# Performance work log

Measured on AMD Instinct MI355X. Metric: run time of the kernel, lower is better.

## Reference

```python
import jax, jax.numpy as jnp
import numpy as np

B, T, F, H, P = 256, 512, 64, 512, 24  # batch, seq_len, fea_dim, hidden, pred_sequence


def setup_inputs() -> dict:
    key = jax.random.key(0)
    ks = jax.random.split(key, 7)
    s = 1.0 / np.sqrt(H)  # PyTorch default init scale
    u = lambda k, shp: jax.random.uniform(k, shp, jnp.float32, -s, s)
    return {
        "x": jax.random.normal(ks[0], (B, T, F), jnp.float32),
        "W_ih": u(ks[1], (4 * H, F)),
        "W_hh": u(ks[2], (4 * H, H)),
        "b_ih": u(ks[3], (4 * H,)),
        "b_hh": u(ks[4], (4 * H,)),
        "W_fc": u(ks[5], (P * F, H)),
        "b_fc": u(ks[6], (P * F,)),
    }


def reference(x, W_ih, W_hh, b_ih, b_hh, W_fc, b_fc):
    b, t, f = x.shape
    h4 = W_hh.shape[1]
    # Precompute input contribution to gates for all timesteps: [B,T,4H]
    x_gates = jnp.einsum('btf,gf->btg', x, W_ih) + b_ih + b_hh

    def step(carry, xg):  # xg: [B,4H]
        h, c = carry
        gates = xg + h @ W_hh.T  # [B,4H]
        i, fg, g, o = jnp.split(gates, 4, axis=-1)  # PyTorch gate order i,f,g,o
        i = jax.nn.sigmoid(i)
        fg = jax.nn.sigmoid(fg)
        o = jax.nn.sigmoid(o)
        g = jnp.tanh(g)
        c = fg * c + i * g
        h = o * jnp.tanh(c)
        return (h, c), None

    h0 = jnp.zeros((b, h4), x.dtype)
    c0 = jnp.zeros((b, h4), x.dtype)
    (hn, cn), _ = jax.lax.scan(step, (h0, c0), jnp.swapaxes(x_gates, 0, 1))
    # hn.squeeze() for num_layers=1 -> [B,H]; fc head then reshape to [B,P,F]
    out = hn @ W_fc.T + b_fc
    return out.reshape(-1, P, f)
```

## Files before the change

### kernel.cpp

```cpp
#include <hip/hip_runtime.h>
#include <stdint.h>


namespace {
constexpr int T_STEPS = 512;
constexpr int FEA  = 64;
constexpr int HID  = 512;
constexpr int NKI  = 18;
constexpr int GSTR = 132;
constexpr int RPG  = 16;
constexpr int GPITCH = 136;
constexpr size_t HBUF_DW  = 256ull * 256;
constexpr size_t FLAG_OFF = 2 * HBUF_DW;
constexpr size_t GRZ_OFF  = FLAG_OFF + 16 * 64;

typedef __bf16   bf16x8 __attribute__((ext_vector_type(8)));
typedef uint16_t u16x8  __attribute__((ext_vector_type(8)));
typedef float    f32x4  __attribute__((ext_vector_type(4)));
typedef uint32_t u32x4  __attribute__((ext_vector_type(4)));

union V8 { u16x8 u; bf16x8 b; u32x4 q; };

__device__ __forceinline__ float bf2f(uint16_t u) {
  union { uint32_t i; float f; } v; v.i = (uint32_t)u << 16; return v.f;
}
__device__ __forceinline__ uint16_t f2bf(float f) {
  union { float f; uint32_t i; } v; v.f = f;
  uint32_t x = v.i;
  return (uint16_t)((x + 0x7FFFu + ((x >> 16) & 1u)) >> 16);
}
__device__ __forceinline__ float sigmoid_f(float x) {
  return 1.0f / (1.0f + __expf(-x));
}
__device__ __forceinline__ float tanh_f(float x) {
  float e = __expf(-2.0f * fabsf(x));
  float t = (1.0f - e) / (1.0f + e);
  return copysignf(t, x);
}
__device__ __forceinline__ bf16x8 load8(const void* base, size_t elem_off,
                                        bool fp32m) {
  V8 r;
  if (fp32m) {
    const float* p = (const float*)base + elem_off;
#pragma unroll
    for (int i = 0; i < 8; ++i) r.u[i] = f2bf(p[i]);
  } else {
    r.q = *(const u32x4*)((const uint16_t*)base + elem_off);
  }
  return r.b;
}
__device__ __forceinline__ float loadf(const void* base, int idx, bool fp32m) {
  return fp32m ? ((const float*)base)[idx] : bf2f(((const uint16_t*)base)[idx]);
}
__device__ __forceinline__ uint2 ldx4(const void* x, size_t elem_off,
                                      bool fp32m) {
  if (fp32m) {
    float4 v = *(const float4*)((const float*)x + elem_off);
    uint2 w;
    w.x = (uint32_t)f2bf(v.x) | ((uint32_t)f2bf(v.y) << 16);
    w.y = (uint32_t)f2bf(v.z) | ((uint32_t)f2bf(v.w) << 16);
    return w;
  }
  return *(const uint2*)((const uint16_t*)x + elem_off);
}

__device__ __forceinline__ u32x4 ld128_sc01(const uint32_t* p) {
  u32x4 v;
  asm volatile("global_load_dwordx4 %0, %1, off sc0 sc1"
               : "=v"(v) : "v"(p) : "memory");
  return v;
}
__device__ __forceinline__ void st32_x(uint32_t* p, uint32_t v, bool xl) {
  if (xl) asm volatile("global_store_dword %0, %1, off sc0"
                       :: "v"(p), "v"(v) : "memory");
  else    asm volatile("global_store_dword %0, %1, off sc0 sc1"
                       :: "v"(p), "v"(v) : "memory");
}
__device__ __forceinline__ void waitcnt_vm0() {
  asm volatile("s_waitcnt vmcnt(0)" ::: "memory");
}
__device__ __forceinline__ void waitcnt_vm0_fence() {
  asm volatile("s_waitcnt vmcnt(0)" ::: "memory");
  __builtin_amdgcn_sched_barrier(0);
}
}

__global__ __launch_bounds__(256, 1) void lstm_persistent(
    const void* __restrict__ x,
    const void* __restrict__ W_ih,
    const void* __restrict__ W_hh,
    const void* __restrict__ b_ih,
    const void* __restrict__ b_hh,
    const void* __restrict__ W_fc,
    const void* __restrict__ b_fc,
    void* __restrict__ out,
    uint32_t* __restrict__ dbuf)
{
  __shared__ __align__(16) uint16_t Als[72 * GPITCH];
  __shared__ float Gls[RPG * GSTR];
  __shared__ int   sflag, sok;

  const int tid = threadIdx.x;
  const int wv  = tid >> 6;
  const int ln  = tid & 63;
  const int nl  = ln & 15;
  const int kq  = ln >> 4;
  const int bg  = blockIdx.x & 15;
  const int wgi = blockIdx.x >> 4;
  const int r0  = bg * RPG;

  if (tid == 0) {
    uint32_t xcc;
    asm volatile("s_getreg_b32 %0, hwreg(HW_REG_XCC_ID)" : "=s"(xcc));
    unsigned* gmask = (unsigned*)(dbuf + GRZ_OFF) + bg;
    unsigned* gcnt  = (unsigned*)(dbuf + GRZ_OFF) + 16 + bg;
    atomicOr(gmask, 1u << (xcc & 31));
    __threadfence();
    atomicAdd(gcnt, 1u);
    while (atomicAdd(gcnt, 0u) < 16u) __builtin_amdgcn_s_sleep(1);
    __threadfence();
    unsigned m = atomicOr(gmask, 0u);
    sok = (__popc(m) == 1) ? 1 : 0;
  }

  if (tid == 1) sflag = 0;
  __syncthreads();
  {
    float a = fabsf(bf2f(((const uint16_t*)b_ih)[tid]));
    if (a > 1.0f) atomicOr(&sflag, 1);
  }
  __syncthreads();
  const bool fp32m = (sflag != 0);
  const bool xloc  = (sok != 0);

  bf16x8 breg[2][NKI];
  float  bias[2];
#pragma unroll
  for (int s = 0; s < 2; ++s) {
    int col  = wv * 32 + s * 16 + nl;
    int gate = col & 3;
    int unit = col >> 2;
    int gcol = gate * HID + wgi * 32 + unit;
#pragma unroll
    for (int kk = 0; kk < NKI; ++kk) {
      int k0 = kk * 32 + kq * 8;
      if (k0 < HID)
        breg[s][kk] = load8(W_hh, (size_t)gcol * HID + k0, fp32m);
      else
        breg[s][kk] = load8(W_ih, (size_t)gcol * FEA + (k0 - HID), fp32m);
    }
    bias[s] = loadf(b_ih, gcol, fp32m) + loadf(b_hh, gcol, fp32m);
  }

  const int ar  = tid >> 4;
  const int au  = (tid & 15) * 2;
  const int hdw = (r0 + ar) * 256 + wgi * 16 + (tid & 15);
  float c0 = 0.0f, c1 = 0.0f;

  const int srow = tid >> 4;
  const int sc   = tid & 15;

  uint32_t* flagw = dbuf + FLAG_OFF + bg * 64 + wgi * 4 + wv;
  const uint32_t* fb0 = dbuf + FLAG_OFF + bg * 64;

  {
    u32x4 z = {0, 0, 0, 0};
    for (int i = tid; i < 64 * GPITCH / 8; i += 256)
      *(u32x4*)&Als[i * 8] = z;
  }
  {
    int gx = sc & 7, hf = sc >> 3;
    size_t off = (size_t)(r0 + srow) * (T_STEPS * FEA) + gx * 8 + hf * 4;
    uint2 w = ldx4(x, off, fp32m);
    *(uint2*)&Als[(64 + gx) * GPITCH + srow * 8 + hf * 4] = w;
  }

  for (int t = 0; t < T_STEPS; ++t) {
    __syncthreads();

    f32x4 acc0, acc1;
    acc0[0] = bias[0]; acc0[1] = bias[0]; acc0[2] = bias[0]; acc0[3] = bias[0];
    acc1[0] = bias[1]; acc1[1] = bias[1]; acc1[2] = bias[1]; acc1[3] = bias[1];
#pragma unroll
    for (int kk = 0; kk < NKI; ++kk) {
      bf16x8 a = *(const bf16x8*)&Als[(4 * kk + kq) * GPITCH + nl * 8];
      acc0 = __builtin_amdgcn_mfma_f32_16x16x32_bf16(a, breg[0][kk], acc0, 0, 0, 0);
      acc1 = __builtin_amdgcn_mfma_f32_16x16x32_bf16(a, breg[1][kk], acc1, 0, 0, 0);
    }
#pragma unroll
    for (int r = 0; r < 4; ++r) {
      Gls[(kq * 4 + r) * GSTR + wv * 32 + nl]      = acc0[r];
      Gls[(kq * 4 + r) * GSTR + wv * 32 + 16 + nl] = acc1[r];
    }
    __syncthreads();

    const uint32_t tg = (uint32_t)(t + 1);
    const bool havex = (t + 1 < T_STEPS);

    {
      const f32x4* gp = (const f32x4*)&Gls[ar * GSTR + au * 4];
      f32x4 ga = gp[0], gb = gp[1];
      c0 = sigmoid_f(ga[1]) * c0 + sigmoid_f(ga[0]) * tanh_f(ga[2]);
      float h0 = sigmoid_f(ga[3]) * tanh_f(c0);
      c1 = sigmoid_f(gb[1]) * c1 + sigmoid_f(gb[0]) * tanh_f(gb[2]);
      float h1 = sigmoid_f(gb[3]) * tanh_f(c1);
      uint32_t hp = (uint32_t)f2bf(h0) | ((uint32_t)f2bf(h1) << 16);
      st32_x(dbuf + (size_t)(tg & 1) * HBUF_DW + hdw, hp, xloc);
      waitcnt_vm0();
      if (ln == 0) st32_x(flagw, tg, xloc);
    }

    if (havex) {
      int gx = sc & 7, hf = sc >> 3;
      size_t off = (size_t)(r0 + srow) * (T_STEPS * FEA)
                 + (size_t)(t + 1) * FEA + gx * 8 + hf * 4;
      uint2 w = ldx4(x, off, fp32m);
      *(uint2*)&Als[(64 + gx) * GPITCH + srow * 8 + hf * 4] = w;
    }

    if (tid < 16) {
      const uint32_t* fp = fb0 + tid * 4;
      for (;;) {
        u32x4 f = ld128_sc01(fp);
        waitcnt_vm0_fence();
        uint32_t mn = f[0];
        mn = f[1] < mn ? f[1] : mn;
        mn = f[2] < mn ? f[2] : mn;
        mn = f[3] < mn ? f[3] : mn;
        if (mn >= tg) break;
      }
    }
    __syncthreads();

    if (havex) {
      const uint32_t* src = dbuf + (size_t)(tg & 1) * HBUF_DW
                          + (size_t)(r0 + srow) * 256;
      u32x4 v0 = ld128_sc01(src + (sc + 0)  * 4);
      u32x4 v1 = ld128_sc01(src + (sc + 16) * 4);
      u32x4 v2 = ld128_sc01(src + (sc + 32) * 4);
      u32x4 v3 = ld128_sc01(src + (sc + 48) * 4);
      waitcnt_vm0();
      *(u32x4*)&Als[(sc + 0)  * GPITCH + srow * 8] = v0;
      *(u32x4*)&Als[(sc + 16) * GPITCH + srow * 8] = v1;
      *(u32x4*)&Als[(sc + 32) * GPITCH + srow * 8] = v2;
      *(u32x4*)&Als[(sc + 48) * GPITCH + srow * 8] = v3;
    }
  }

  int gwave = wgi * 4 + wv;
  for (int tile = gwave; tile < 96; tile += 64) {
    int n = tile * 16 + nl;
    float bs = loadf(b_fc, n, fp32m);
    f32x4 acc; acc[0] = bs; acc[1] = bs; acc[2] = bs; acc[3] = bs;
    const uint32_t* hb = dbuf + (size_t)(r0 + nl) * 256 + kq * 4;
    V8 av[16];
#pragma unroll
    for (int p = 0; p < 16; ++p) av[p].q = ld128_sc01(hb + p * 16);
    waitcnt_vm0_fence();
#pragma unroll
    for (int kk = 0; kk < 16; ++kk) {
      bf16x8 b = load8(W_fc, (size_t)n * HID + kk * 32 + kq * 8, fp32m);
      acc = __builtin_amdgcn_mfma_f32_16x16x32_bf16(av[kk].b, b, acc, 0, 0, 0);
    }
#pragma unroll
    for (int r = 0; r < 4; ++r) {
      int row = r0 + kq * 4 + r;
      if (fp32m) ((float*)out)[(size_t)row * 1536 + n] = acc[r];
      else       ((uint16_t*)out)[(size_t)row * 1536 + n] = f2bf(acc[r]);
    }
  }
}

extern "C" void kernel_launch(void* const* d_in, const int* in_sizes, int n_in,
                              void* d_out, int out_size, void* d_ws, size_t ws_size,
                              hipStream_t stream) {
  const void* x    = d_in[0];
  const void* W_ih = d_in[1];
  const void* W_hh = d_in[2];
  const void* b_ih = d_in[3];
  const void* b_hh = d_in[4];
  const void* W_fc = d_in[5];
  const void* b_fc = d_in[6];
  uint32_t* dbuf = (uint32_t*)d_ws;

  hipMemsetAsync((void*)(dbuf + FLAG_OFF), 0,
                 (16 * 64 + 32) * sizeof(uint32_t), stream);

  lstm_persistent<<<dim3(256), dim3(256), 0, stream>>>(
      x, W_ih, W_hh, b_ih, b_hh, W_fc, b_fc, d_out, dbuf);
}
```

Measured before the change: 1.033 ms.

## Per-lane flag polling with direct h-chunk fetch; split MFMA accumulators; fc reads LDS

Result: slower. 1.170 ms (+13.2%).

```diff
diff --git a/kernel.cpp b/kernel.cpp
--- a/kernel.cpp
+++ b/kernel.cpp
@@ -64,6 +64,12 @@
   return *(const uint2*)((const uint16_t*)x + elem_off);
 }
 
+__device__ __forceinline__ uint32_t ld32_sc01(const uint32_t* p) {
+  uint32_t v;
+  asm volatile("global_load_dword %0, %1, off sc0 sc1"
+               : "=v"(v) : "v"(p) : "memory");
+  return v;
+}
 __device__ __forceinline__ u32x4 ld128_sc01(const uint32_t* p) {
   u32x4 v;
   asm volatile("global_load_dwordx4 %0, %1, off sc0 sc1"
@@ -160,8 +166,12 @@
   const int srow = tid >> 4;
   const int sc   = tid & 15;
 
+  const int prow = ln & 15;
+  const int pkk  = wv * 4 + (ln >> 4);
+
   uint32_t* flagw = dbuf + FLAG_OFF + bg * 64 + wgi * 4 + wv;
   const uint32_t* fb0 = dbuf + FLAG_OFF + bg * 64;
+  const uint32_t* pflag = fb0 + pkk * 4 + (prow >> 2);
 
   {
     u32x4 z = {0, 0, 0, 0};
@@ -178,19 +188,27 @@
   for (int t = 0; t < T_STEPS; ++t) {
     __syncthreads();
 
-    f32x4 acc0, acc1;
-    acc0[0] = bias[0]; acc0[1] = bias[0]; acc0[2] = bias[0]; acc0[3] = bias[0];
-    acc1[0] = bias[1]; acc1[1] = bias[1]; acc1[2] = bias[1]; acc1[3] = bias[1];
+    f32x4 c0a, c0b, c1a, c1b;
+#pragma unroll
+    for (int i = 0; i < 4; ++i) {
+      c0a[i] = bias[0]; c1a[i] = bias[1]; c0b[i] = 0.0f; c1b[i] = 0.0f;
+    }
 #pragma unroll
     for (int kk = 0; kk < NKI; ++kk) {
       bf16x8 a = *(const bf16x8*)&Als[(4 * kk + kq) * GPITCH + nl * 8];
-      acc0 = __builtin_amdgcn_mfma_f32_16x16x32_bf16(a, breg[0][kk], acc0, 0, 0, 0);
-      acc1 = __builtin_amdgcn_mfma_f32_16x16x32_bf16(a, breg[1][kk], acc1, 0, 0, 0);
-    }
+      if (kk & 1) {
+        c0b = __builtin_amdgcn_mfma_f32_16x16x32_bf16(a, breg[0][kk], c0b, 0, 0, 0);
+        c1b = __builtin_amdgcn_mfma_f32_16x16x32_bf16(a, breg[1][kk], c1b, 0, 0, 0);
+      } else {
+        c0a = __builtin_amdgcn_mfma_f32_16x16x32_bf16(a, breg[0][kk], c0a, 0, 0, 0);
+        c1a = __builtin_amdgcn_mfma_f32_16x16x32_bf16(a, breg[1][kk], c1a, 0, 0, 0);
+      }
+    }
+    f32x4 A0 = c0a + c0b, A1 = c1a + c1b;
 #pragma unroll
     for (int r = 0; r < 4; ++r) {
-      Gls[(kq * 4 + r) * GSTR + wv * 32 + nl]      = acc0[r];
-      Gls[(kq * 4 + r) * GSTR + wv * 32 + 16 + nl] = acc1[r];
+      Gls[(kq * 4 + r) * GSTR + wv * 32 + nl]      = A0[r];
+      Gls[(kq * 4 + r) * GSTR + wv * 32 + 16 + nl] = A1[r];
     }
     __syncthreads();
 
@@ -218,49 +236,38 @@
       *(uint2*)&Als[(64 + gx) * GPITCH + srow * 8 + hf * 4] = w;
     }
 
-    if (tid < 16) {
-      const uint32_t* fp = fb0 + tid * 4;
+    {
       for (;;) {
-        u32x4 f = ld128_sc01(fp);
+        uint32_t f = ld32_sc01(pflag);
         waitcnt_vm0_fence();
-        uint32_t mn = f[0];
-        mn = f[1] < mn ? f[1] : mn;
-        mn = f[2] < mn ? f[2] : mn;
-        mn = f[3] < mn ? f[3] : mn;
-        if (mn >= tg) break;
+        if (f >= tg) break;
       }
-    }
-    __syncthreads();
-
-    if (havex) {
       const uint32_t* src = dbuf + (size_t)(tg & 1) * HBUF_DW
-                          + (size_t)(r0 + srow) * 256;
-      u32x4 v0 = ld128_sc01(src + (sc + 0)  * 4);
-      u32x4 v1 = ld128_sc01(src + (sc + 16) * 4);
-      u32x4 v2 = ld128_sc01(src + (sc + 32) * 4);
-      u32x4 v3 = ld128_sc01(src + (sc + 48) * 4);
+                          + (size_t)(r0 + prow) * 256 + pkk * 16;
+      u32x4 v0 = ld128_sc01(src + 0);
+      u32x4 v1 = ld128_sc01(src + 4);
+      u32x4 v2 = ld128_sc01(src + 8);
+      u32x4 v3 = ld128_sc01(src + 12);
       waitcnt_vm0();
-      *(u32x4*)&Als[(sc + 0)  * GPITCH + srow * 8] = v0;
-      *(u32x4*)&Als[(sc + 16) * GPITCH + srow * 8] = v1;
-      *(u32x4*)&Als[(sc + 32) * GPITCH + srow * 8] = v2;
-      *(u32x4*)&Als[(sc + 48) * GPITCH + srow * 8] = v3;
-    }
-  }
+      uint16_t* d = &Als[(pkk * 4) * GPITCH + prow * 8];
+      *(u32x4*)(d + 0 * GPITCH) = v0;
+      *(u32x4*)(d + 1 * GPITCH) = v1;
+      *(u32x4*)(d + 2 * GPITCH) = v2;
+      *(u32x4*)(d + 3 * GPITCH) = v3;
+    }
+  }
+  __syncthreads();
 
   int gwave = wgi * 4 + wv;
   for (int tile = gwave; tile < 96; tile += 64) {
     int n = tile * 16 + nl;
     float bs = loadf(b_fc, n, fp32m);
     f32x4 acc; acc[0] = bs; acc[1] = bs; acc[2] = bs; acc[3] = bs;
-    const uint32_t* hb = dbuf + (size_t)(r0 + nl) * 256 + kq * 4;
-    V8 av[16];
-#pragma unroll
-    for (int p = 0; p < 16; ++p) av[p].q = ld128_sc01(hb + p * 16);
-    waitcnt_vm0_fence();
 #pragma unroll
     for (int kk = 0; kk < 16; ++kk) {
+      bf16x8 a = *(const bf16x8*)&Als[(4 * kk + kq) * GPITCH + nl * 8];
       bf16x8 b = load8(W_fc, (size_t)n * HID + kk * 32 + kq * 8, fp32m);
-      acc = __builtin_amdgcn_mfma_f32_16x16x32_bf16(av[kk].b, b, acc, 0, 0, 0);
+      acc = __builtin_amdgcn_mfma_f32_16x16x32_bf16(a, b, acc, 0, 0, 0);
     }
 #pragma unroll
     for (int r = 0; r < 4; ++r) {
```

## Double-buffer LDS A tile and drop per-step block barriers in LSTM recurrence

Applied to the files above, without the earlier changes.

Result: faster. 1.003 ms (-3.0%).

```diff
diff --git a/kernel.cpp b/kernel.cpp
--- a/kernel.cpp
+++ b/kernel.cpp
@@ -7,8 +7,7 @@
 constexpr int FEA  = 64;
 constexpr int HID  = 512;
 constexpr int NKI  = 18;
-constexpr int GSTR = 132;
-constexpr int RPG  = 16;
+constexpr int GWS  = 36;
 constexpr int GPITCH = 136;
 constexpr size_t HBUF_DW  = 256ull * 256;
 constexpr size_t FLAG_OFF = 2 * HBUF_DW;
@@ -64,6 +63,12 @@
   return *(const uint2*)((const uint16_t*)x + elem_off);
 }
 
+__device__ __forceinline__ uint32_t ld32_sc01(const uint32_t* p) {
+  uint32_t v;
+  asm volatile("global_load_dword %0, %1, off sc0 sc1"
+               : "=v"(v) : "v"(p) : "memory");
+  return v;
+}
 __device__ __forceinline__ u32x4 ld128_sc01(const uint32_t* p) {
   u32x4 v;
   asm volatile("global_load_dwordx4 %0, %1, off sc0 sc1"
@@ -96,8 +101,8 @@
     void* __restrict__ out,
     uint32_t* __restrict__ dbuf)
 {
-  __shared__ __align__(16) uint16_t Als[72 * GPITCH];
-  __shared__ float Gls[RPG * GSTR];
+  __shared__ __align__(16) uint16_t Als[2][72 * GPITCH];
+  __shared__ float Gw[4][16 * GWS];
   __shared__ int   sflag, sok;
 
   const int tid = threadIdx.x;
@@ -107,7 +112,7 @@
   const int kq  = ln >> 4;
   const int bg  = blockIdx.x & 15;
   const int wgi = blockIdx.x >> 4;
-  const int r0  = bg * RPG;
+  const int r0  = bg * 16;
 
   if (tid == 0) {
     uint32_t xcc;
@@ -152,54 +157,59 @@
     bias[s] = loadf(b_ih, gcol, fp32m) + loadf(b_hh, gcol, fp32m);
   }
 
-  const int ar  = tid >> 4;
-  const int au  = (tid & 15) * 2;
-  const int hdw = (r0 + ar) * 256 + wgi * 16 + (tid & 15);
+  const int arow = ln >> 2;
+  const int up   = ln & 3;
+  const int hdw  = (r0 + arow) * 256 + wgi * 16 + wv * 4 + up;
   float c0 = 0.0f, c1 = 0.0f;
 
   const int srow = tid >> 4;
   const int sc   = tid & 15;
 
   uint32_t* flagw = dbuf + FLAG_OFF + bg * 64 + wgi * 4 + wv;
-  const uint32_t* fb0 = dbuf + FLAG_OFF + bg * 64;
+  const uint32_t* fbase = dbuf + FLAG_OFF + bg * 64;
 
   {
     u32x4 z = {0, 0, 0, 0};
     for (int i = tid; i < 64 * GPITCH / 8; i += 256)
-      *(u32x4*)&Als[i * 8] = z;
+      *(u32x4*)&Als[0][i * 8] = z;
   }
   {
     int gx = sc & 7, hf = sc >> 3;
     size_t off = (size_t)(r0 + srow) * (T_STEPS * FEA) + gx * 8 + hf * 4;
     uint2 w = ldx4(x, off, fp32m);
-    *(uint2*)&Als[(64 + gx) * GPITCH + srow * 8 + hf * 4] = w;
+    *(uint2*)&Als[0][(64 + gx) * GPITCH + srow * 8 + hf * 4] = w;
   }
 
   for (int t = 0; t < T_STEPS; ++t) {
     __syncthreads();
+
+    const uint16_t* Ar = &Als[t & 1][0];
+    uint16_t*       Aw = &Als[(t + 1) & 1][0];
 
     f32x4 acc0, acc1;
     acc0[0] = bias[0]; acc0[1] = bias[0]; acc0[2] = bias[0]; acc0[3] = bias[0];
     acc1[0] = bias[1]; acc1[1] = bias[1]; acc1[2] = bias[1]; acc1[3] = bias[1];
 #pragma unroll
     for (int kk = 0; kk < NKI; ++kk) {
-      bf16x8 a = *(const bf16x8*)&Als[(4 * kk + kq) * GPITCH + nl * 8];
+      bf16x8 a = *(const bf16x8*)&Ar[(4 * kk + kq) * GPITCH + nl * 8];
       acc0 = __builtin_amdgcn_mfma_f32_16x16x32_bf16(a, breg[0][kk], acc0, 0, 0, 0);
       acc1 = __builtin_amdgcn_mfma_f32_16x16x32_bf16(a, breg[1][kk], acc1, 0, 0, 0);
     }
+
+    float* G = &Gw[wv][0];
 #pragma unroll
     for (int r = 0; r < 4; ++r) {
-      Gls[(kq * 4 + r) * GSTR + wv * 32 + nl]      = acc0[r];
-      Gls[(kq * 4 + r) * GSTR + wv * 32 + 16 + nl] = acc1[r];
-    }
-    __syncthreads();
+      G[(kq * 4 + r) * GWS + nl]      = acc0[r];
+      G[(kq * 4 + r) * GWS + 16 + nl] = acc1[r];
+    }
 
     const uint32_t tg = (uint32_t)(t + 1);
     const bool havex = (t + 1 < T_STEPS);
 
     {
-      const f32x4* gp = (const f32x4*)&Gls[ar * GSTR + au * 4];
-      f32x4 ga = gp[0], gb = gp[1];
+      const float* gp = &Gw[wv][arow * GWS + up * 8];
+      f32x4 ga = *(const f32x4*)gp;
+      f32x4 gb = *(const f32x4*)(gp + 4);
       c0 = sigmoid_f(ga[1]) * c0 + sigmoid_f(ga[0]) * tanh_f(ga[2]);
       float h0 = sigmoid_f(ga[3]) * tanh_f(c0);
       c1 = sigmoid_f(gb[1]) * c1 + sigmoid_f(gb[0]) * tanh_f(gb[2]);
@@ -215,24 +225,17 @@
       size_t off = (size_t)(r0 + srow) * (T_STEPS * FEA)
                  + (size_t)(t + 1) * FEA + gx * 8 + hf * 4;
       uint2 w = ldx4(x, off, fp32m);
-      *(uint2*)&Als[(64 + gx) * GPITCH + srow * 8 + hf * 4] = w;
-    }
-
-    if (tid < 16) {
-      const uint32_t* fp = fb0 + tid * 4;
-      for (;;) {
-        u32x4 f = ld128_sc01(fp);
-        waitcnt_vm0_fence();
-        uint32_t mn = f[0];
-        mn = f[1] < mn ? f[1] : mn;
-        mn = f[2] < mn ? f[2] : mn;
-        mn = f[3] < mn ? f[3] : mn;
-        if (mn >= tg) break;
-      }
-    }
-    __syncthreads();
-
-    if (havex) {
+      *(uint2*)&Aw[(64 + gx) * GPITCH + srow * 8 + hf * 4] = w;
+    }
+
+    for (;;) {
+      uint32_t f = ld32_sc01(fbase + ln);
+      waitcnt_vm0_fence();
+      if (f >= tg) break;
+      __builtin_amdgcn_s_sleep(1);
+    }
+
+    {
       const uint32_t* src = dbuf + (size_t)(tg & 1) * HBUF_DW
                           + (size_t)(r0 + srow) * 256;
       u32x4 v0 = ld128_sc01(src + (sc + 0)  * 4);
@@ -240,27 +243,24 @@
       u32x4 v2 = ld128_sc01(src + (sc + 32) * 4);
       u32x4 v3 = ld128_sc01(src + (sc + 48) * 4);
       waitcnt_vm0();
-      *(u32x4*)&Als[(sc + 0)  * GPITCH + srow * 8] = v0;
-      *(u32x4*)&Als[(sc + 16) * GPITCH + srow * 8] = v1;
-      *(u32x4*)&Als[(sc + 32) * GPITCH + srow * 8] = v2;
-      *(u32x4*)&Als[(sc + 48) * GPITCH + srow * 8] = v3;
-    }
-  }
+      *(u32x4*)&Aw[(sc + 0)  * GPITCH + srow * 8] = v0;
+      *(u32x4*)&Aw[(sc + 16) * GPITCH + srow * 8] = v1;
+      *(u32x4*)&Aw[(sc + 32) * GPITCH + srow * 8] = v2;
+      *(u32x4*)&Aw[(sc + 48) * GPITCH + srow * 8] = v3;
+    }
+  }
+  __syncthreads();
 
   int gwave = wgi * 4 + wv;
   for (int tile = gwave; tile < 96; tile += 64) {
     int n = tile * 16 + nl;
     float bs = loadf(b_fc, n, fp32m);
     f32x4 acc; acc[0] = bs; acc[1] = bs; acc[2] = bs; acc[3] = bs;
-    const uint32_t* hb = dbuf + (size_t)(r0 + nl) * 256 + kq * 4;
-    V8 av[16];
-#pragma unroll
-    for (int p = 0; p < 16; ++p) av[p].q = ld128_sc01(hb + p * 16);
-    waitcnt_vm0_fence();
 #pragma unroll
     for (int kk = 0; kk < 16; ++kk) {
+      bf16x8 a = *(const bf16x8*)&Als[0][(4 * kk + kq) * GPITCH + nl * 8];
       bf16x8 b = load8(W_fc, (size_t)n * HID + kk * 32 + kq * 8, fp32m);
-      acc = __builtin_amdgcn_mfma_f32_16x16x32_bf16(av[kk].b, b, acc, 0, 0, 0);
+      acc = __builtin_amdgcn_mfma_f32_16x16x32_bf16(a, b, acc, 0, 0, 0);
     }
 #pragma unroll
     for (int r = 0; r < 4; ++r) {
```
